# Performance work log

Hardware: AMD Instinct MI355X
Metric: run time of the kernel (lower is better)

## Reference

```python
import jax, jax.numpy as jnp
import numpy as np

NEG_INF = -1e9  # matches masked_fill value -1000000000.0
LEAKY_SLOPE = 0.2


def setup_inputs() -> dict:
    key = jax.random.key(0)
    k1, k2, k3, k4 = jax.random.split(key, 4)
    B, N, D_in, D_out = 8, 2048, 256, 256
    x = jax.random.normal(k1, (B, N, D_in), dtype=jnp.float32)
    adj_matrix = jax.random.randint(k2, (B, N, N), 0, 2, dtype=jnp.int32)
    # torch nn.Linear weights: W is [out, in], attention a is [1, 2*out]
    W = jax.random.normal(k3, (D_out, D_in), dtype=jnp.float32) / np.sqrt(D_in)
    a = jax.random.normal(k4, (1, 2 * D_out), dtype=jnp.float32) / np.sqrt(2 * D_out)
    return {"x": x, "adj_matrix": adj_matrix, "W": W, "a": a}


def reference(x, adj_matrix, W, a):
    # h = W(x): [B, N, D_out]
    h = jnp.einsum('bnd,od->bno', x, W)
    D = h.shape[-1]
    # attention(concat(h_i, h_j)) == h_i @ a_left + h_j @ a_right (bias-free linear)
    a_left, a_right = a[0, :D], a[0, D:]
    e = (h @ a_left)[:, :, None] + (h @ a_right)[:, None, :]  # [B, N, N]
    e = jnp.where(e > 0, e, LEAKY_SLOPE * e)  # LeakyReLU(0.2)
    e = jnp.where(adj_matrix == 0, NEG_INF, e)
    alpha = jax.nn.softmax(e, axis=-1)
    return jnp.einsum('bij,bjd->bid', alpha, h)
```

## Files before the change

kernel.cpp:

```cpp
#include <hip/hip_runtime.h>
#include <hip/hip_bf16.h>

typedef __attribute__((ext_vector_type(8))) __bf16 bf16x8;
typedef __attribute__((ext_vector_type(4))) float f32x4;
typedef __attribute__((ext_vector_type(4))) int int4v;

#define NB 8
#define NN 2048
#define ND 256

__global__ __launch_bounds__(256) void k2_elr(
    const float* __restrict__ x, const float* __restrict__ W,
    const float* __restrict__ a, float* __restrict__ el,
    float* __restrict__ er) {
  __shared__ float wls[ND], wrs[ND];
  int t = threadIdx.x;
  {
    float swl = 0.f, swr = 0.f;
    for (int o = 0; o < ND; ++o) {
      float wv = W[(long)o * ND + t];
      swl = fmaf(a[o], wv, swl);
      swr = fmaf(a[ND + o], wv, swr);
    }
    wls[t] = swl;
    wrs[t] = swr;
  }
  __syncthreads();
  int r = t >> 2, q = t & 3;
  long row = (long)blockIdx.x * 64 + r;
  const f32x4* xr = (const f32x4*)(x + row * ND);
  float sl = 0.f, sr = 0.f;
#pragma unroll
  for (int ii = 0; ii < 16; ++ii) {
    int idx = q + (ii << 2);
    f32x4 xv = xr[idx];
    f32x4 lv = *(const f32x4*)(wls + idx * 4);
    f32x4 rv = *(const f32x4*)(wrs + idx * 4);
    sl += xv[0] * lv[0] + xv[1] * lv[1] + xv[2] * lv[2] + xv[3] * lv[3];
    sr += xv[0] * rv[0] + xv[1] * rv[1] + xv[2] * rv[2] + xv[3] * rv[3];
  }
  sl += __shfl_xor(sl, 1);
  sl += __shfl_xor(sl, 2);
  sr += __shfl_xor(sr, 1);
  sr += __shfl_xor(sr, 2);
  if (q == 0) {
    el[row] = sl;
    er[row] = sr;
  }
}

__global__ __launch_bounds__(256) void k1_h(
    const float* __restrict__ x, const float* __restrict__ W,
    __bf16* __restrict__ hT) {
  __shared__ __bf16 hlds[256 * 34];
  int tid = threadIdx.x;
  int wid = tid >> 6, lane = tid & 63;
  int msub = wid & 1, nh = wid >> 1;
  int lrow = lane & 15, kg = lane >> 4;
  int m0 = blockIdx.x * 32;
  int row = m0 + msub * 16 + lrow;

  f32x4 acc[8];
#pragma unroll
  for (int f = 0; f < 8; ++f) acc[f] = (f32x4){0.f, 0.f, 0.f, 0.f};

#pragma unroll
  for (int k0 = 0; k0 < ND; k0 += 32) {
    int kk = k0 + kg * 8;
    const f32x4* xa = (const f32x4*)(x + (long)row * ND + kk);
    f32x4 a0 = xa[0], a1 = xa[1];
    bf16x8 afrag;
    afrag[0] = (__bf16)a0[0]; afrag[1] = (__bf16)a0[1];
    afrag[2] = (__bf16)a0[2]; afrag[3] = (__bf16)a0[3];
    afrag[4] = (__bf16)a1[0]; afrag[5] = (__bf16)a1[1];
    afrag[6] = (__bf16)a1[2]; afrag[7] = (__bf16)a1[3];
#pragma unroll
    for (int f = 0; f < 8; ++f) {
      int o = nh * 128 + f * 16 + lrow;
      const f32x4* wb = (const f32x4*)(W + (long)o * ND + kk);
      f32x4 b0 = wb[0], b1 = wb[1];
      bf16x8 bfrag;
      bfrag[0] = (__bf16)b0[0]; bfrag[1] = (__bf16)b0[1];
      bfrag[2] = (__bf16)b0[2]; bfrag[3] = (__bf16)b0[3];
      bfrag[4] = (__bf16)b1[0]; bfrag[5] = (__bf16)b1[1];
      bfrag[6] = (__bf16)b1[2]; bfrag[7] = (__bf16)b1[3];
      acc[f] = __builtin_amdgcn_mfma_f32_16x16x32_bf16(afrag, bfrag, acc[f], 0, 0, 0);
    }
  }

#pragma unroll
  for (int f = 0; f < 8; ++f) {
    int d = nh * 128 + f * 16 + lrow;
#pragma unroll
    for (int r = 0; r < 4; ++r) {
      int nloc = msub * 16 + kg * 4 + r;
      hlds[d * 34 + nloc] = (__bf16)acc[f][r];
    }
  }
  __syncthreads();
  {
    int b = m0 >> 11;
    int n0 = m0 & (NN - 1);
    const int* src = (const int*)(hlds + tid * 34);
    int tmp[16];
#pragma unroll
    for (int j = 0; j < 16; ++j) tmp[j] = src[j];
    __bf16* dst = hT + ((long)b * ND + tid) * NN + n0;
#pragma unroll
    for (int j = 0; j < 4; ++j)
      *(int4v*)(dst + j * 8) = *(int4v*)(tmp + j * 4);
  }
}

__global__ __launch_bounds__(256, 2) void k3_main(
    const int* __restrict__ adj, const __bf16* __restrict__ hT,
    const float* __restrict__ el, const float* __restrict__ er,
    float* __restrict__ out) {
  __shared__ __bf16 hbuf[3][256 * 32];
  __shared__ int abuf[3][32 * 32];
  __shared__ float er_lds[NN];

  int blk = blockIdx.x;
  int b = blk & 7;
  int it = blk >> 3;
  int tid = threadIdx.x;
  int wid = tid >> 6, lane = tid & 63;
  int isub = wid & 1, dh = wid >> 1;
  int lrow = lane & 15, kg = lane >> 4;
  int irow = it * 32 + isub * 16 + lrow;

  const __bf16* hTb = hT + (long)b * ND * NN;
  const float* erb = er + (long)b * NN;
  const int* adjb = adj + ((long)b * NN + (long)it * 32) * NN;

  {
    f32x4 e0 = *(const f32x4*)(erb + tid * 8);
    f32x4 e1 = *(const f32x4*)(erb + tid * 8 + 4);
    *(f32x4*)(er_lds + tid * 8) = e0;
    *(f32x4*)(er_lds + tid * 8 + 4) = e1;
  }
  float eli = el[b * NN + irow];
  float el16 = eli + 16.0f;

  auto stage = [&](int s, int tc) {
    const __bf16* hsrc = hTb + tc * 32;
    __bf16* hdst = &hbuf[s][0];
#pragma unroll
    for (int r = 0; r < 4; ++r) {
      int idx = r * 256 + tid;
      int d = idx >> 2;
      int g = (idx & 3) ^ ((d & 3) ^ ((d >> 2) & 3));
      __builtin_amdgcn_global_load_lds(
          (const __attribute__((address_space(1))) void*)(hsrc + (long)d * NN + g * 8),
          (__attribute__((address_space(3))) void*)(hdst + idx * 8), 16, 0, 0);
    }
    int r2 = tid >> 3;
    int g2 = (tid & 7) ^ (r2 & 7);
    __builtin_amdgcn_global_load_lds(
        (const __attribute__((address_space(1))) void*)(adjb + (long)r2 * NN + tc * 32 + g2 * 4),
        (__attribute__((address_space(3))) void*)(&abuf[s][0] + tid * 4), 16, 0, 0);
  };

  f32x4 acc[8];
#pragma unroll
  for (int f = 0; f < 8; ++f) acc[f] = (f32x4){0.f, 0.f, 0.f, 0.f};
  float den = 0.f;

  int d_base = dh * 128 + lrow;
  int hsw = (lrow & 3) ^ ((lrow >> 2) & 3);
  int hoff = d_base * 64 + ((kg ^ hsw) << 4);
  int rloc = isub * 16 + lrow;
  int swa = rloc & 7;
  int aoff0 = rloc * 128 + (((kg * 2) ^ swa) << 4);
  int aoff1 = rloc * 128 + (((kg * 2 + 1) ^ swa) << 4);

  stage(0, 0);
  stage(1, 1);
  __syncthreads();

  for (int tc = 0; tc < 64; ++tc) {
    if (tc < 63)
      asm volatile("s_waitcnt vmcnt(5)" ::: "memory");
    else
      asm volatile("s_waitcnt vmcnt(0)" ::: "memory");
    __builtin_amdgcn_s_barrier();
    asm volatile("" ::: "memory");
    if (tc + 2 < 64) stage((tc + 2) % 3, tc + 2);

    int cb = tc % 3;
    const char* ab = (const char*)(&abuf[cb][0]);
    int4v a0 = *(const int4v*)(ab + aoff0);
    int4v a1 = *(const int4v*)(ab + aoff1);
    f32x4 ea = *(const f32x4*)(er_lds + tc * 32 + kg * 8);
    f32x4 eb = *(const f32x4*)(er_lds + tc * 32 + kg * 8 + 4);

    bf16x8 pfrag;
    float ps = 0.f;
#pragma unroll
    for (int e = 0; e < 8; ++e) {
      int aj = (e < 4) ? a0[e] : a1[e - 4];
      float erx = (e < 4) ? ea[e] : eb[e - 4];
      float z = eli + erx;
      float s = fmaxf(z, 0.2f * z);
      float p = __expf(s - el16);
      p = (aj != 0) ? p : 0.0f;
      ps += p;
      pfrag[e] = (__bf16)p;
    }
    den += ps;

    const char* hb = (const char*)(&hbuf[cb][0]);
#pragma unroll
    for (int f = 0; f < 8; ++f) {
      bf16x8 bfr = *(const bf16x8*)(hb + hoff + f * 1024);
      acc[f] = __builtin_amdgcn_mfma_f32_16x16x32_bf16(pfrag, bfr, acc[f], 0, 0, 0);
    }
  }

  den += __shfl_xor(den, 16);
  den += __shfl_xor(den, 32);
  float rdiv[4];
#pragma unroll
  for (int r = 0; r < 4; ++r) rdiv[r] = 1.0f / __shfl(den, kg * 4 + r);

  float* outb = out + ((long)b * NN + it * 32 + isub * 16) * ND;
#pragma unroll
  for (int f = 0; f < 8; ++f) {
    int dcol = d_base + f * 16;
#pragma unroll
    for (int r = 0; r < 4; ++r)
      outb[(long)(kg * 4 + r) * ND + dcol] = acc[f][r] * rdiv[r];
  }
}

extern "C" void kernel_launch(void* const* d_in, const int* in_sizes, int n_in,
                              void* d_out, int out_size, void* d_ws,
                              size_t ws_size, hipStream_t stream) {
  const float* x = (const float*)d_in[0];
  const int* adj = (const int*)d_in[1];
  const float* W = (const float*)d_in[2];
  const float* a = (const float*)d_in[3];
  float* out = (float*)d_out;

  char* ws = (char*)d_ws;
  const size_t base = 8u * 1024u * 1024u;
  __bf16* hT = (__bf16*)ws;
  float* el = (float*)(ws + base);
  float* er = (float*)(ws + base + 65536u);

  k1_h<<<dim3(512), dim3(256), 0, stream>>>(x, W, hT);
  k2_elr<<<dim3(256), dim3(256), 0, stream>>>(x, W, a, el, er);
  k3_main<<<dim3(512), dim3(256), 0, stream>>>(adj, hT, el, er, out);
}
```

Measured before the change: 107.0 us.

## Precompute exp2-domain logit terms and load adjacency directly to registers

The el/er projection kernel now emits pre-scaled log2-domain terms, so the main loop computes each attention weight with a single max and exp2, with no leaky-relu or subtraction. In the main kernel, adjacency and er values are loaded per lane straight from global memory into registers, replacing the LDS staging. The loop is unrolled by three with explicit triple buffering, uses a revised h-tile swizzle, and raises wave priority around the MFMAs. Direct global loads of adjacency may coalesce less well than the LDS path.

New measurement: 127.2 us. 1.19x slower.

```diff
diff --git a/kernel.cpp b/kernel.cpp
--- a/kernel.cpp
+++ b/kernel.cpp
@@ -8,11 +8,12 @@
 #define NB 8
 #define NN 2048
 #define ND 256
+#define L2E 1.44269504f
 
 __global__ __launch_bounds__(256) void k2_elr(
     const float* __restrict__ x, const float* __restrict__ W,
-    const float* __restrict__ a, float* __restrict__ el,
-    float* __restrict__ er) {
+    const float* __restrict__ a, float* __restrict__ elc,
+    float* __restrict__ er2) {
   __shared__ float wls[ND], wrs[ND];
   int t = threadIdx.x;
   {
@@ -44,8 +45,11 @@
   sr += __shfl_xor(sr, 1);
   sr += __shfl_xor(sr, 2);
   if (q == 0) {
-    el[row] = sl;
-    er[row] = sr;
+    elc[row] = (-0.8f * sl - 16.0f) * L2E;
+    float2 v;
+    v.x = (sr - 16.0f) * L2E;
+    v.y = 0.2f * sr * L2E;
+    *(float2*)(er2 + row * 2) = v;
   }
 }
 
@@ -114,11 +118,9 @@
 
 __global__ __launch_bounds__(256, 2) void k3_main(
     const int* __restrict__ adj, const __bf16* __restrict__ hT,
-    const float* __restrict__ el, const float* __restrict__ er,
+    const float* __restrict__ elc, const float* __restrict__ er2,
     float* __restrict__ out) {
   __shared__ __bf16 hbuf[3][256 * 32];
-  __shared__ int abuf[3][32 * 32];
-  __shared__ float er_lds[NN];
 
   int blk = blockIdx.x;
   int b = blk & 7;
@@ -130,92 +132,120 @@
   int irow = it * 32 + isub * 16 + lrow;
 
   const __bf16* hTb = hT + (long)b * ND * NN;
-  const float* erb = er + (long)b * NN;
-  const int* adjb = adj + ((long)b * NN + (long)it * 32) * NN;
-
-  {
-    f32x4 e0 = *(const f32x4*)(erb + tid * 8);
-    f32x4 e1 = *(const f32x4*)(erb + tid * 8 + 4);
-    *(f32x4*)(er_lds + tid * 8) = e0;
-    *(f32x4*)(er_lds + tid * 8 + 4) = e1;
-  }
-  float eli = el[b * NN + irow];
-  float el16 = eli + 16.0f;
-
-  auto stage = [&](int s, int tc) {
-    const __bf16* hsrc = hTb + tc * 32;
-    __bf16* hdst = &hbuf[s][0];
-#pragma unroll
-    for (int r = 0; r < 4; ++r) {
-      int idx = r * 256 + tid;
-      int d = idx >> 2;
-      int g = (idx & 3) ^ ((d & 3) ^ ((d >> 2) & 3));
-      __builtin_amdgcn_global_load_lds(
-          (const __attribute__((address_space(1))) void*)(hsrc + (long)d * NN + g * 8),
-          (__attribute__((address_space(3))) void*)(hdst + idx * 8), 16, 0, 0);
-    }
-    int r2 = tid >> 3;
-    int g2 = (tid & 7) ^ (r2 & 7);
-    __builtin_amdgcn_global_load_lds(
-        (const __attribute__((address_space(1))) void*)(adjb + (long)r2 * NN + tc * 32 + g2 * 4),
-        (__attribute__((address_space(3))) void*)(&abuf[s][0] + tid * 4), 16, 0, 0);
-  };
+  const int* adjrow = adj + ((long)b * NN + irow) * NN;
+  const float* er2b = er2 + (long)b * NN * 2;
+  float c1s = elc[b * NN + irow];
+  int kg8 = kg * 8;
+
+  int d0 = tid >> 2;
+  int spp = tid & 3;
+  int jlog = (spp ^ ((d0 >> 1) & 3)) * 8;
+  const __bf16* sbase = hTb + (long)d0 * NN + jlog;
+
+  int sp_r = kg ^ ((lrow >> 1) & 3);
+  int hoff = (dh * 128 + lrow) * 64 + sp_r * 16;
+  int d_base = dh * 128 + lrow;
 
   f32x4 acc[8];
 #pragma unroll
   for (int f = 0; f < 8; ++f) acc[f] = (f32x4){0.f, 0.f, 0.f, 0.f};
   float den = 0.f;
 
-  int d_base = dh * 128 + lrow;
-  int hsw = (lrow & 3) ^ ((lrow >> 2) & 3);
-  int hoff = d_base * 64 + ((kg ^ hsw) << 4);
-  int rloc = isub * 16 + lrow;
-  int swa = rloc & 7;
-  int aoff0 = rloc * 128 + (((kg * 2) ^ swa) << 4);
-  int aoff1 = rloc * 128 + (((kg * 2 + 1) ^ swa) << 4);
-
-  stage(0, 0);
-  stage(1, 1);
-  __syncthreads();
-
-  for (int tc = 0; tc < 64; ++tc) {
-    if (tc < 63)
-      asm volatile("s_waitcnt vmcnt(5)" ::: "memory");
-    else
-      asm volatile("s_waitcnt vmcnt(0)" ::: "memory");
-    __builtin_amdgcn_s_barrier();
-    asm volatile("" ::: "memory");
-    if (tc + 2 < 64) stage((tc + 2) % 3, tc + 2);
-
-    int cb = tc % 3;
-    const char* ab = (const char*)(&abuf[cb][0]);
-    int4v a0 = *(const int4v*)(ab + aoff0);
-    int4v a1 = *(const int4v*)(ab + aoff1);
-    f32x4 ea = *(const f32x4*)(er_lds + tc * 32 + kg * 8);
-    f32x4 eb = *(const f32x4*)(er_lds + tc * 32 + kg * 8 + 4);
-
-    bf16x8 pfrag;
-    float ps = 0.f;
-#pragma unroll
-    for (int e = 0; e < 8; ++e) {
-      int aj = (e < 4) ? a0[e] : a1[e - 4];
-      float erx = (e < 4) ? ea[e] : eb[e - 4];
-      float z = eli + erx;
-      float s = fmaxf(z, 0.2f * z);
-      float p = __expf(s - el16);
-      p = (aj != 0) ? p : 0.0f;
-      ps += p;
-      pfrag[e] = (__bf16)p;
-    }
-    den += ps;
-
-    const char* hb = (const char*)(&hbuf[cb][0]);
-#pragma unroll
-    for (int f = 0; f < 8; ++f) {
-      bf16x8 bfr = *(const bf16x8*)(hb + hoff + f * 1024);
-      acc[f] = __builtin_amdgcn_mfma_f32_16x16x32_bf16(pfrag, bfr, acc[f], 0, 0, 0);
-    }
-  }
+  int4v aj0_0, aj1_0, aj0_1, aj1_1, aj0_2, aj1_2;
+  f32x4 e0_0, e1_0, e2_0, e3_0;
+  f32x4 e0_1, e1_1, e2_1, e3_1;
+  f32x4 e0_2, e1_2, e2_2, e3_2;
+
+#define STAGEH(BI, TCV)                                                       \
+  {                                                                           \
+    const __bf16* s0 = sbase + (TCV)*32;                                      \
+    _Pragma("unroll") for (int rr = 0; rr < 4; ++rr) {                        \
+      __builtin_amdgcn_global_load_lds(                                       \
+          (const __attribute__((address_space(1))) void*)(s0 + (long)rr * 64 * NN), \
+          (__attribute__((address_space(3))) void*)(&hbuf[BI][0] +            \
+                                                    (rr * 256 + tid) * 8),    \
+          16, 0, 0);                                                          \
+    }                                                                         \
+  }
+
+#define LOADSET(S, TCV)                                                       \
+  {                                                                           \
+    const int* ap = adjrow + (TCV)*32 + kg8;                                  \
+    aj0_##S = *(const int4v*)(ap);                                            \
+    aj1_##S = *(const int4v*)(ap + 4);                                        \
+    const float* ep = er2b + ((TCV)*32 + kg8) * 2;                            \
+    e0_##S = *(const f32x4*)(ep);                                             \
+    e1_##S = *(const f32x4*)(ep + 4);                                         \
+    e2_##S = *(const f32x4*)(ep + 8);                                         \
+    e3_##S = *(const f32x4*)(ep + 12);                                        \
+  }
+
+#define COMPUTE(BI, S)                                                        \
+  {                                                                           \
+    bf16x8 pfrag;                                                             \
+    float ps = 0.f;                                                           \
+    _Pragma("unroll") for (int e = 0; e < 8; ++e) {                           \
+      f32x4 ev = (e < 2) ? e0_##S : (e < 4) ? e1_##S : (e < 6) ? e2_##S : e3_##S; \
+      float x16 = ev[(e & 1) * 2];                                            \
+      float x02 = ev[(e & 1) * 2 + 1];                                        \
+      int aj = (e < 4) ? aj0_##S[e] : aj1_##S[e & 3];                         \
+      float m = fmaxf(x16, x02 + c1s);                                        \
+      float p = __builtin_amdgcn_exp2f(m);                                    \
+      p = aj ? p : 0.0f;                                                      \
+      ps += p;                                                                \
+      pfrag[e] = (__bf16)p;                                                   \
+    }                                                                         \
+    den += ps;                                                                \
+    const char* hb = (const char*)&hbuf[BI][0];                               \
+    __builtin_amdgcn_s_setprio(1);                                            \
+    _Pragma("unroll") for (int f = 0; f < 8; ++f) {                           \
+      bf16x8 bfr = *(const bf16x8*)(hb + hoff + f * 1024);                    \
+      acc[f] = __builtin_amdgcn_mfma_f32_16x16x32_bf16(pfrag, bfr, acc[f], 0, 0, 0); \
+    }                                                                         \
+    __builtin_amdgcn_s_setprio(0);                                            \
+  }
+
+#define WAITB(VMN)                                            \
+  asm volatile("s_waitcnt vmcnt(" VMN ")" ::: "memory");      \
+  __builtin_amdgcn_s_barrier();
+
+  LOADSET(0, 0);
+  STAGEH(0, 0);
+  LOADSET(1, 1);
+  STAGEH(1, 1);
+
+  for (int t3 = 0; t3 < 20; ++t3) {
+    int tc = t3 * 3;
+    WAITB("10");
+    STAGEH(2, tc + 2);
+    LOADSET(2, tc + 2);
+    COMPUTE(0, 0);
+    WAITB("10");
+    STAGEH(0, tc + 3);
+    LOADSET(0, tc + 3);
+    COMPUTE(1, 1);
+    WAITB("10");
+    STAGEH(1, tc + 4);
+    LOADSET(1, tc + 4);
+    COMPUTE(2, 2);
+  }
+  WAITB("10");
+  STAGEH(2, 62);
+  LOADSET(2, 62);
+  COMPUTE(0, 0);
+  WAITB("10");
+  STAGEH(0, 63);
+  LOADSET(0, 63);
+  COMPUTE(1, 1);
+  WAITB("10");
+  COMPUTE(2, 2);
+  WAITB("0");
+  COMPUTE(0, 0);
+
+#undef STAGEH
+#undef LOADSET
+#undef COMPUTE
+#undef WAITB
 
   den += __shfl_xor(den, 16);
   den += __shfl_xor(den, 32);
@@ -245,10 +275,10 @@
   char* ws = (char*)d_ws;
   const size_t base = 8u * 1024u * 1024u;
   __bf16* hT = (__bf16*)ws;
-  float* el = (float*)(ws + base);
-  float* er = (float*)(ws + base + 65536u);
+  float* elc = (float*)(ws + base);
+  float* er2 = (float*)(ws + base + 65536u);
 
   k1_h<<<dim3(512), dim3(256), 0, stream>>>(x, W, hT);
-  k2_elr<<<dim3(256), dim3(256), 0, stream>>>(x, W, a, el, er);
-  k3_main<<<dim3(512), dim3(256), 0, stream>>>(adj, hT, el, er, out);
-}
+  k2_elr<<<dim3(256), dim3(256), 0, stream>>>(x, W, a, elc, er2);
+  k3_main<<<dim3(512), dim3(256), 0, stream>>>(adj, hT, elc, er2, out);
+}
```
